# Kernel optimization log

Measured on AMD Instinct MI355X. Metric: run time of the kernel, lower is better.

Reference implementation:

```python
import jax, jax.numpy as jnp
import numpy as np

DIM = 1024
N_HEADS = 16
HEAD_DIM = DIM // N_HEADS
D_LATENT = 256
B, T = 1, 4096


def setup_inputs() -> dict:
    key = jax.random.key(0)
    ks = jax.random.split(key, 6)
    s = 0.02
    return {
        "x": jax.random.normal(ks[0], (B, T, DIM), dtype=jnp.float32),
        "W_DKV": jax.random.normal(ks[1], (DIM, D_LATENT), dtype=jnp.float32) * s,
        "W_UK": jax.random.normal(ks[2], (D_LATENT, DIM), dtype=jnp.float32) * s,
        "W_UV": jax.random.normal(ks[3], (D_LATENT, DIM), dtype=jnp.float32) * s,
        "W_UQ": jax.random.normal(ks[4], (DIM, DIM), dtype=jnp.float32) * s,
        "W_O": jax.random.normal(ks[5], (DIM, DIM), dtype=jnp.float32) * s,
    }


def reference(x, W_DKV, W_UK, W_UV, W_UQ, W_O):
    b, t, d = x.shape
    h, hd = N_HEADS, HEAD_DIM
    # low-rank latent KV projection
    c_kv = x @ W_DKV                                   # (b, t, d_latent)
    k = (c_kv @ W_UK).reshape(b, t, h, hd)             # (b, t, h, hd)
    v = (c_kv @ W_UV).reshape(b, t, h, hd)
    q = (x @ W_UQ).reshape(b, t, h, hd)
    scale = 1.0 / jnp.sqrt(jnp.asarray(hd, x.dtype))
    scores = jnp.einsum("bqhd,bkhd->bhqk", q, k) * scale   # (b, h, t, t)
    causal = jnp.tril(jnp.ones((t, t), dtype=bool))
    scores = jnp.where(causal, scores, jnp.asarray(-jnp.inf, scores.dtype))
    probs = jax.nn.softmax(scores, axis=-1)            # dropout is eval-mode identity
    ctx = jnp.einsum("bhqk,bkhd->bqhd", probs, v).reshape(b, t, d)
    return ctx @ W_O
```

## Files before the change

### kernel.cpp

```cpp
#include <hip/hip_runtime.h>
#include <hip/hip_bf16.h>
#include <stdint.h>

#define T_SEQ 4096
#define DIMX 1024
#define NH 16
#define HD 64
#define DLAT 256

typedef __bf16 bf16x8 __attribute__((ext_vector_type(8)));
typedef __bf16 bf16x4 __attribute__((ext_vector_type(4)));
typedef float floatx4 __attribute__((ext_vector_type(4)));

#define MFMA(a, b, c) __builtin_amdgcn_mfma_f32_16x16x32_bf16(a, b, c, 0, 0, 0)

__device__ inline void gload_lds16(const __bf16* g, __bf16* l) {
  __builtin_amdgcn_global_load_lds(
      (const __attribute__((address_space(1))) uint32_t*)g,
      (__attribute__((address_space(3))) uint32_t*)l, 16, 0, 0);
}

__global__ __launch_bounds__(256) void prep_kernel(
    const float* __restrict__ x, const float* __restrict__ wdkv,
    const float* __restrict__ wuk, const float* __restrict__ wuv,
    const float* __restrict__ wuq, const float* __restrict__ wo,
    __bf16* __restrict__ x_bf, __bf16* __restrict__ wt_dkv,
    __bf16* __restrict__ wt_uk, __bf16* __restrict__ wt_uv,
    __bf16* __restrict__ wt_uq, __bf16* __restrict__ wt_o) {
  int id = blockIdx.x;
  if (id < 2048) {
    int i = id * 256 + threadIdx.x;
    const float4* p = (const float4*)x;
    float4 a = p[2 * i], b = p[2 * i + 1];
    bf16x8 r = {(__bf16)a.x, (__bf16)a.y, (__bf16)a.z, (__bf16)a.w,
                (__bf16)b.x, (__bf16)b.y, (__bf16)b.z, (__bf16)b.w};
    *(bf16x8*)(x_bf + 8 * (size_t)i) = r;
    return;
  }
  int t = id - 2048;
  const float* in;
  __bf16* out;
  int R, C, lt;
  if (t < 64)       { in = wdkv; out = wt_dkv; R = 1024; C = 256;  lt = t; }
  else if (t < 128) { in = wuk;  out = wt_uk;  R = 256;  C = 1024; lt = t - 64; }
  else if (t < 192) { in = wuv;  out = wt_uv;  R = 256;  C = 1024; lt = t - 128; }
  else if (t < 448) { in = wuq;  out = wt_uq;  R = 1024; C = 1024; lt = t - 192; }
  else              { in = wo;   out = wt_o;   R = 1024; C = 1024; lt = t - 448; }
  __shared__ __bf16 tls[64][65];
  int tpr = C >> 6;
  int r0 = (lt / tpr) * 64, c0 = (lt % tpr) * 64;
  int tid = threadIdx.x;
#pragma unroll
  for (int i = 0; i < 16; i++) {
    int idx = tid + i * 256;
    int r = idx >> 6, c = idx & 63;
    tls[r][c] = (__bf16)in[(size_t)(r0 + r) * C + c0 + c];
  }
  __syncthreads();
#pragma unroll
  for (int i = 0; i < 16; i++) {
    int idx = tid + i * 256;
    int rr = idx & 63, cc = idx >> 6;
    out[(size_t)(c0 + cc) * R + r0 + rr] = tls[rr][cc];
  }
}

#define BUFE 4096

__global__ __launch_bounds__(256) void gemm_a128(const __bf16* __restrict__ A,
                                                 const __bf16* __restrict__ B1,
                                                 const __bf16* __restrict__ B2,
                                                 __bf16* __restrict__ C1,
                                                 __bf16* __restrict__ C2) {
  __shared__ __attribute__((aligned(16))) __bf16 Al[2][BUFE];
  __shared__ __attribute__((aligned(16))) __bf16 Bl[2][BUFE];
  int tid = threadIdx.x;
  int w = tid >> 6, lane = tid & 63;
  int quad = lane >> 4, l16 = lane & 15;
  int mw = w & 1, nw = w >> 1;
  int bx = blockIdx.x, m0 = blockIdx.y * 128;
  const __bf16* Bt;
  __bf16* C;
  int n0, N;
  float sc;
  if (bx < 2) { Bt = B1; C = C1; n0 = bx * 128; N = DLAT; sc = 1.0f; }
  else        { Bt = B2; C = C2; n0 = (bx - 2) * 128; N = DIMX;
                sc = 0.125f * 1.44269504088896340736f; }
  const int K = DIMX;
  int arow = w * 32 + (lane >> 2), acol = (lane & 3) << 3;

  floatx4 acc[4][4];
#pragma unroll
  for (int i = 0; i < 4; i++)
#pragma unroll
    for (int j = 0; j < 4; j++) acc[i][j] = (floatx4){0.f, 0.f, 0.f, 0.f};

  for (int k0 = 0; k0 < K; k0 += 64) {
#pragma unroll
    for (int kh = 0; kh < 2; kh++)
#pragma unroll
      for (int j = 0; j < 2; j++) {
        gload_lds16(A + (size_t)(m0 + arow + j * 16) * K + k0 + kh * 32 + acol,
                    &Al[kh][(w * 32 + j * 16) * 32]);
        gload_lds16(Bt + (size_t)(n0 + arow + j * 16) * K + k0 + kh * 32 + acol,
                    &Bl[kh][(w * 32 + j * 16) * 32]);
      }
    __syncthreads();
#pragma unroll
    for (int kh = 0; kh < 2; kh++) {
      bf16x8 af[4], bfr[4];
#pragma unroll
      for (int mt = 0; mt < 4; mt++)
        af[mt] =
            *(const bf16x8*)&Al[kh][(mw * 64 + mt * 16 + l16) * 32 + quad * 8];
#pragma unroll
      for (int nt = 0; nt < 4; nt++)
        bfr[nt] =
            *(const bf16x8*)&Bl[kh][(nw * 64 + nt * 16 + l16) * 32 + quad * 8];
#pragma unroll
      for (int mt = 0; mt < 4; mt++)
#pragma unroll
        for (int nt = 0; nt < 4; nt++)
          acc[mt][nt] = MFMA(af[mt], bfr[nt], acc[mt][nt]);
    }
    __syncthreads();
  }
#pragma unroll
  for (int mt = 0; mt < 4; mt++)
#pragma unroll
    for (int nt = 0; nt < 4; nt++)
#pragma unroll
      for (int r = 0; r < 4; r++) {
        int row = m0 + mw * 64 + mt * 16 + quad * 4 + r;
        int col = n0 + nw * 64 + nt * 16 + l16;
        C[(size_t)row * N + col] = (__bf16)(acc[mt][nt][r] * sc);
      }
}

__global__ __launch_bounds__(256) void gemm_kv128(const __bf16* __restrict__ A,
                                                  const __bf16* __restrict__ Bk,
                                                  const __bf16* __restrict__ Bv,
                                                  __bf16* __restrict__ k,
                                                  __bf16* __restrict__ vt) {
  __shared__ __attribute__((aligned(16))) __bf16 Al[2][BUFE];
  __shared__ __attribute__((aligned(16))) __bf16 Bl[2][BUFE];
  __shared__ __attribute__((aligned(16))) __bf16 tw[4][64 * 72];
  int tid = threadIdx.x;
  int w = tid >> 6, lane = tid & 63;
  int quad = lane >> 4, l16 = lane & 15;
  int mw = w & 1, nw = w >> 1;
  int bx = blockIdx.x, m0 = blockIdx.y * 128;
  bool is_k = (bx < 8);
  const __bf16* Bt = is_k ? Bk : Bv;
  int n0 = (is_k ? bx : bx - 8) * 128;
  const int K = DLAT;
  int arow = w * 32 + (lane >> 2), acol = (lane & 3) << 3;

  floatx4 acc[4][4];
#pragma unroll
  for (int i = 0; i < 4; i++)
#pragma unroll
    for (int j = 0; j < 4; j++) acc[i][j] = (floatx4){0.f, 0.f, 0.f, 0.f};

  for (int k0 = 0; k0 < K; k0 += 64) {
#pragma unroll
    for (int kh = 0; kh < 2; kh++)
#pragma unroll
      for (int j = 0; j < 2; j++) {
        gload_lds16(A + (size_t)(m0 + arow + j * 16) * K + k0 + kh * 32 + acol,
                    &Al[kh][(w * 32 + j * 16) * 32]);
        gload_lds16(Bt + (size_t)(n0 + arow + j * 16) * K + k0 + kh * 32 + acol,
                    &Bl[kh][(w * 32 + j * 16) * 32]);
      }
    __syncthreads();
#pragma unroll
    for (int kh = 0; kh < 2; kh++) {
      bf16x8 af[4], bfr[4];
#pragma unroll
      for (int mt = 0; mt < 4; mt++)
        af[mt] =
            *(const bf16x8*)&Al[kh][(mw * 64 + mt * 16 + l16) * 32 + quad * 8];
#pragma unroll
      for (int nt = 0; nt < 4; nt++)
        bfr[nt] =
            *(const bf16x8*)&Bl[kh][(nw * 64 + nt * 16 + l16) * 32 + quad * 8];
#pragma unroll
      for (int mt = 0; mt < 4; mt++)
#pragma unroll
        for (int nt = 0; nt < 4; nt++)
          acc[mt][nt] = MFMA(af[mt], bfr[nt], acc[mt][nt]);
    }
    __syncthreads();
  }
  if (is_k) {
#pragma unroll
    for (int mt = 0; mt < 4; mt++)
#pragma unroll
      for (int nt = 0; nt < 4; nt++)
#pragma unroll
        for (int r = 0; r < 4; r++) {
          int row = m0 + mw * 64 + mt * 16 + quad * 4 + r;
          int col = n0 + nw * 64 + nt * 16 + l16;
          k[(size_t)row * DIMX + col] = (__bf16)acc[mt][nt][r];
        }
  } else {
#pragma unroll
    for (int mt = 0; mt < 4; mt++)
#pragma unroll
      for (int nt = 0; nt < 4; nt++)
#pragma unroll
        for (int r = 0; r < 4; r++)
          tw[w][(nt * 16 + l16) * 72 + mt * 16 + quad * 4 + r] =
              (__bf16)acc[mt][nt][r];
    int cbase = lane >> 3, chunk = lane & 7;
#pragma unroll
    for (int i = 0; i < 8; i++) {
      int c = cbase + i * 8;
      bf16x8 v8 = *(const bf16x8*)&tw[w][c * 72 + chunk * 8];
      *(bf16x8*)&vt[(size_t)(n0 + nw * 64 + c) * T_SEQ + m0 + mw * 64 +
                    chunk * 8] = v8;
    }
  }
}

__global__ __launch_bounds__(256) void gemm_f128(const __bf16* __restrict__ A,
                                                 const __bf16* __restrict__ Bt,
                                                 float* __restrict__ C) {
  __shared__ __attribute__((aligned(16))) __bf16 Al[2][BUFE];
  __shared__ __attribute__((aligned(16))) __bf16 Bl[2][BUFE];
  int tid = threadIdx.x;
  int w = tid >> 6, lane = tid & 63;
  int quad = lane >> 4, l16 = lane & 15;
  int mw = w & 1, nw = w >> 1;
  int n0 = blockIdx.x * 128, m0 = blockIdx.y * 128;
  const int K = DIMX, N = DIMX;
  int arow = w * 32 + (lane >> 2), acol = (lane & 3) << 3;

  floatx4 acc[4][4];
#pragma unroll
  for (int i = 0; i < 4; i++)
#pragma unroll
    for (int j = 0; j < 4; j++) acc[i][j] = (floatx4){0.f, 0.f, 0.f, 0.f};

  for (int k0 = 0; k0 < K; k0 += 64) {
#pragma unroll
    for (int kh = 0; kh < 2; kh++)
#pragma unroll
      for (int j = 0; j < 2; j++) {
        gload_lds16(A + (size_t)(m0 + arow + j * 16) * K + k0 + kh * 32 + acol,
                    &Al[kh][(w * 32 + j * 16) * 32]);
        gload_lds16(Bt + (size_t)(n0 + arow + j * 16) * K + k0 + kh * 32 + acol,
                    &Bl[kh][(w * 32 + j * 16) * 32]);
      }
    __syncthreads();
#pragma unroll
    for (int kh = 0; kh < 2; kh++) {
      bf16x8 af[4], bfr[4];
#pragma unroll
      for (int mt = 0; mt < 4; mt++)
        af[mt] =
            *(const bf16x8*)&Al[kh][(mw * 64 + mt * 16 + l16) * 32 + quad * 8];
#pragma unroll
      for (int nt = 0; nt < 4; nt++)
        bfr[nt] =
            *(const bf16x8*)&Bl[kh][(nw * 64 + nt * 16 + l16) * 32 + quad * 8];
#pragma unroll
      for (int mt = 0; mt < 4; mt++)
#pragma unroll
        for (int nt = 0; nt < 4; nt++)
          acc[mt][nt] = MFMA(af[mt], bfr[nt], acc[mt][nt]);
    }
    __syncthreads();
  }
#pragma unroll
  for (int mt = 0; mt < 4; mt++)
#pragma unroll
    for (int nt = 0; nt < 4; nt++)
#pragma unroll
      for (int r = 0; r < 4; r++) {
        int row = m0 + mw * 64 + mt * 16 + quad * 4 + r;
        int col = n0 + nw * 64 + nt * 16 + l16;
        C[(size_t)row * N + col] = acc[mt][nt][r];
      }
}

#define PST 72
__global__ __launch_bounds__(256, 3) void mla_attn8(const __bf16* __restrict__ Q,
                                                    const __bf16* __restrict__ Kg,
                                                    const __bf16* __restrict__ Vt,
                                                    __bf16* __restrict__ ctx) {
  __shared__ __attribute__((aligned(16))) __bf16 Kl[2][64 * 64];
  __shared__ __attribute__((aligned(16))) __bf16 Vl[2][64 * 64];
  __shared__ __attribute__((aligned(16))) __bf16 Pl[64 * PST];
  int tid = threadIdx.x;
  int wave = tid >> 6, lane = tid & 63;
  int quad = lane >> 4, l16 = lane & 15;
  int h = blockIdx.y;
  int qt = 63 - blockIdx.x;
  int q0 = qt * 64;
  int srow = tid >> 3, pos = tid & 7;
  int gco = pos << 3;
  int sw = (pos ^ (srow & 7)) << 3;
  int swr = srow * 64 + sw;
  int fr = (wave * 16 + l16) * PST;
  int c0s = ((quad ^ (l16 & 7)) << 3);
  int c1s = (((4 + quad) ^ (l16 & 7)) << 3);

  *(bf16x8*)&Pl[srow * PST + gco] =
      *(const bf16x8*)&Q[(size_t)(q0 + srow) * DIMX + h * HD + gco];
  *(bf16x8*)&Pl[(srow + 32) * PST + gco] =
      *(const bf16x8*)&Q[(size_t)(q0 + srow + 32) * DIMX + h * HD + gco];
  *(bf16x8*)&Kl[0][swr] =
      *(const bf16x8*)&Kg[(size_t)srow * DIMX + h * HD + gco];
  *(bf16x8*)&Kl[0][swr + 2048] =
      *(const bf16x8*)&Kg[(size_t)(srow + 32) * DIMX + h * HD + gco];
  *(bf16x8*)&Vl[0][swr] =
      *(const bf16x8*)&Vt[(size_t)(h * HD + srow) * T_SEQ + gco];
  *(bf16x8*)&Vl[0][swr + 2048] =
      *(const bf16x8*)&Vt[(size_t)(h * HD + srow + 32) * T_SEQ + gco];
  __syncthreads();
  bf16x8 qf0 = *(const bf16x8*)&Pl[fr + quad * 8];
  bf16x8 qf1 = *(const bf16x8*)&Pl[fr + 32 + quad * 8];

  floatx4 o[4];
  float lsum = 0.f;
#pragma unroll
  for (int i = 0; i < 4; i++) o[i] = (floatx4){0.f, 0.f, 0.f, 0.f};

  for (int kt = 0; kt <= qt; kt++) {
    int cur = kt & 1, nxt = cur ^ 1;
    bool pre = (kt < qt);
    bf16x8 kp0, kp1, vp0, vp1;
    if (pre) {
      int k0n = (kt + 1) * 64;
      kp0 = *(const bf16x8*)&Kg[(size_t)(k0n + srow) * DIMX + h * HD + gco];
      kp1 = *(const bf16x8*)&Kg[(size_t)(k0n + srow + 32) * DIMX + h * HD + gco];
      vp0 = *(const bf16x8*)&Vt[(size_t)(h * HD + srow) * T_SEQ + k0n + gco];
      vp1 = *(const bf16x8*)&Vt[(size_t)(h * HD + srow + 32) * T_SEQ + k0n + gco];
    }
    const __bf16* Kc = Kl[cur];
    const __bf16* Vc = Vl[cur];
    floatx4 s[4];
    __builtin_amdgcn_s_setprio(1);
#pragma unroll
    for (int ct = 0; ct < 4; ct++) {
      int rb = (ct * 16 + l16) * 64;
      bf16x8 kf0 = *(const bf16x8*)&Kc[rb + c0s];
      bf16x8 kf1 = *(const bf16x8*)&Kc[rb + c1s];
      floatx4 z = (floatx4){0.f, 0.f, 0.f, 0.f};
      z = MFMA(kf0, qf0, z);
      z = MFMA(kf1, qf1, z);
      s[ct] = z;
    }
    __builtin_amdgcn_s_setprio(0);
    bool diag = (kt == qt);
#pragma unroll
    for (int ct = 0; ct < 4; ct++) {
      float p0[4];
#pragma unroll
      for (int r = 0; r < 4; r++) {
        float p = __builtin_amdgcn_exp2f(s[ct][r]);
        if (diag && (ct * 16 + quad * 4 + r > wave * 16 + l16)) p = 0.f;
        lsum += p;
        p0[r] = p;
      }
      bf16x4 pk = {(__bf16)p0[0], (__bf16)p0[1], (__bf16)p0[2], (__bf16)p0[3]};
      *(bf16x4*)&Pl[(wave * 16 + l16) * PST + ct * 16 + quad * 4] = pk;
    }
    bf16x8 pf0 = *(const bf16x8*)&Pl[fr + quad * 8];
    bf16x8 pf1 = *(const bf16x8*)&Pl[fr + 32 + quad * 8];
    __builtin_amdgcn_s_setprio(1);
#pragma unroll
    for (int dt = 0; dt < 4; dt++) {
      int rb = (dt * 16 + l16) * 64;
      bf16x8 vf0 = *(const bf16x8*)&Vc[rb + c0s];
      bf16x8 vf1 = *(const bf16x8*)&Vc[rb + c1s];
      o[dt] = MFMA(pf0, vf0, o[dt]);
      o[dt] = MFMA(pf1, vf1, o[dt]);
    }
    __builtin_amdgcn_s_setprio(0);
    if (pre) {
      *(bf16x8*)&Kl[nxt][swr] = kp0;
      *(bf16x8*)&Kl[nxt][swr + 2048] = kp1;
      *(bf16x8*)&Vl[nxt][swr] = vp0;
      *(bf16x8*)&Vl[nxt][swr + 2048] = vp1;
    }
    __syncthreads();
  }

  lsum += __shfl_xor(lsum, 16, 64);
  lsum += __shfl_xor(lsum, 32, 64);
  float inv[4];
#pragma unroll
  for (int r = 0; r < 4; r++) inv[r] = 1.0f / __shfl(lsum, quad * 4 + r, 16);

#pragma unroll
  for (int dt = 0; dt < 4; dt++)
#pragma unroll
    for (int r = 0; r < 4; r++) {
      float val = o[dt][r] * inv[r];
      int row = q0 + wave * 16 + quad * 4 + r;
      int col = h * HD + dt * 16 + l16;
      ctx[(size_t)row * DIMX + col] = (__bf16)val;
    }
}

extern "C" void kernel_launch(void* const* d_in, const int* in_sizes, int n_in,
                              void* d_out, int out_size, void* d_ws,
                              size_t ws_size, hipStream_t stream) {
  const float* x = (const float*)d_in[0];
  const float* wdkv = (const float*)d_in[1];
  const float* wuk = (const float*)d_in[2];
  const float* wuv = (const float*)d_in[3];
  const float* wuq = (const float*)d_in[4];
  const float* wo = (const float*)d_in[5];
  float* out = (float*)d_out;

  __bf16* ws = (__bf16*)d_ws;
  __bf16* x_bf = ws;
  __bf16* q = x_bf + (size_t)T_SEQ * DIMX;
  __bf16* k = q + (size_t)T_SEQ * DIMX;
  __bf16* vt = k + (size_t)T_SEQ * DIMX;
  __bf16* ctx = vt + (size_t)T_SEQ * DIMX;
  __bf16* ckv = ctx + (size_t)T_SEQ * DIMX;
  __bf16* wt_dkv = ckv + (size_t)T_SEQ * DLAT;
  __bf16* wt_uk = wt_dkv + (size_t)DLAT * DIMX;
  __bf16* wt_uv = wt_uk + (size_t)DIMX * DLAT;
  __bf16* wt_uq = wt_uv + (size_t)DIMX * DLAT;
  __bf16* wt_o = wt_uq + (size_t)DIMX * DIMX;

  dim3 blk(256);
  prep_kernel<<<dim3(2752), blk, 0, stream>>>(x, wdkv, wuk, wuv, wuq, wo, x_bf,
                                              wt_dkv, wt_uk, wt_uv, wt_uq, wt_o);
  gemm_a128<<<dim3(10, T_SEQ / 128), blk, 0, stream>>>(x_bf, wt_dkv, wt_uq,
                                                       ckv, q);
  gemm_kv128<<<dim3(16, T_SEQ / 128), blk, 0, stream>>>(ckv, wt_uk, wt_uv, k,
                                                        vt);
  mla_attn8<<<dim3(64, NH), dim3(256), 0, stream>>>(q, k, vt, ctx);
  gemm_f128<<<dim3(DIMX / 128, T_SEQ / 128), blk, 0, stream>>>(ctx, wt_o, out);
}
```

Measured before the change: 229.1 us.

## Load V fragments from global into registers and swap attention grid order

```diff
diff --git a/kernel.cpp b/kernel.cpp
--- a/kernel.cpp
+++ b/kernel.cpp
@@ -285,18 +285,17 @@
 }
 
 #define PST 72
-__global__ __launch_bounds__(256, 3) void mla_attn8(const __bf16* __restrict__ Q,
+__global__ __launch_bounds__(256, 3) void mla_attn9(const __bf16* __restrict__ Q,
                                                     const __bf16* __restrict__ Kg,
                                                     const __bf16* __restrict__ Vt,
                                                     __bf16* __restrict__ ctx) {
   __shared__ __attribute__((aligned(16))) __bf16 Kl[2][64 * 64];
-  __shared__ __attribute__((aligned(16))) __bf16 Vl[2][64 * 64];
   __shared__ __attribute__((aligned(16))) __bf16 Pl[64 * PST];
   int tid = threadIdx.x;
   int wave = tid >> 6, lane = tid & 63;
   int quad = lane >> 4, l16 = lane & 15;
-  int h = blockIdx.y;
-  int qt = 63 - blockIdx.x;
+  int h = blockIdx.x;
+  int qt = 63 - blockIdx.y;
   int q0 = qt * 64;
   int srow = tid >> 3, pos = tid & 7;
   int gco = pos << 3;
@@ -305,6 +304,7 @@
   int fr = (wave * 16 + l16) * PST;
   int c0s = ((quad ^ (l16 & 7)) << 3);
   int c1s = (((4 + quad) ^ (l16 & 7)) << 3);
+  const __bf16* vptr = Vt + (size_t)(h * HD + l16) * T_SEQ + quad * 8;
 
   *(bf16x8*)&Pl[srow * PST + gco] =
       *(const bf16x8*)&Q[(size_t)(q0 + srow) * DIMX + h * HD + gco];
@@ -314,10 +314,13 @@
       *(const bf16x8*)&Kg[(size_t)srow * DIMX + h * HD + gco];
   *(bf16x8*)&Kl[0][swr + 2048] =
       *(const bf16x8*)&Kg[(size_t)(srow + 32) * DIMX + h * HD + gco];
-  *(bf16x8*)&Vl[0][swr] =
-      *(const bf16x8*)&Vt[(size_t)(h * HD + srow) * T_SEQ + gco];
-  *(bf16x8*)&Vl[0][swr + 2048] =
-      *(const bf16x8*)&Vt[(size_t)(h * HD + srow + 32) * T_SEQ + gco];
+  bf16x8 vc[8], vn[8];
+#pragma unroll
+  for (int dt = 0; dt < 4; dt++)
+#pragma unroll
+    for (int hf = 0; hf < 2; hf++)
+      vc[dt * 2 + hf] =
+          *(const bf16x8*)&vptr[(size_t)(dt * 16) * T_SEQ + hf * 32];
   __syncthreads();
   bf16x8 qf0 = *(const bf16x8*)&Pl[fr + quad * 8];
   bf16x8 qf1 = *(const bf16x8*)&Pl[fr + 32 + quad * 8];
@@ -330,16 +333,19 @@
   for (int kt = 0; kt <= qt; kt++) {
     int cur = kt & 1, nxt = cur ^ 1;
     bool pre = (kt < qt);
-    bf16x8 kp0, kp1, vp0, vp1;
+    bf16x8 kp0, kp1;
     if (pre) {
       int k0n = (kt + 1) * 64;
       kp0 = *(const bf16x8*)&Kg[(size_t)(k0n + srow) * DIMX + h * HD + gco];
       kp1 = *(const bf16x8*)&Kg[(size_t)(k0n + srow + 32) * DIMX + h * HD + gco];
-      vp0 = *(const bf16x8*)&Vt[(size_t)(h * HD + srow) * T_SEQ + k0n + gco];
-      vp1 = *(const bf16x8*)&Vt[(size_t)(h * HD + srow + 32) * T_SEQ + k0n + gco];
+#pragma unroll
+      for (int dt = 0; dt < 4; dt++)
+#pragma unroll
+        for (int hf = 0; hf < 2; hf++)
+          vn[dt * 2 + hf] = *(const bf16x8*)&vptr[(size_t)(dt * 16) * T_SEQ +
+                                                  k0n + hf * 32];
     }
     const __bf16* Kc = Kl[cur];
-    const __bf16* Vc = Vl[cur];
     floatx4 s[4];
     __builtin_amdgcn_s_setprio(1);
 #pragma unroll
@@ -372,18 +378,15 @@
     __builtin_amdgcn_s_setprio(1);
 #pragma unroll
     for (int dt = 0; dt < 4; dt++) {
-      int rb = (dt * 16 + l16) * 64;
-      bf16x8 vf0 = *(const bf16x8*)&Vc[rb + c0s];
-      bf16x8 vf1 = *(const bf16x8*)&Vc[rb + c1s];
-      o[dt] = MFMA(pf0, vf0, o[dt]);
-      o[dt] = MFMA(pf1, vf1, o[dt]);
+      o[dt] = MFMA(pf0, vc[dt * 2 + 0], o[dt]);
+      o[dt] = MFMA(pf1, vc[dt * 2 + 1], o[dt]);
     }
     __builtin_amdgcn_s_setprio(0);
     if (pre) {
       *(bf16x8*)&Kl[nxt][swr] = kp0;
       *(bf16x8*)&Kl[nxt][swr + 2048] = kp1;
-      *(bf16x8*)&Vl[nxt][swr] = vp0;
-      *(bf16x8*)&Vl[nxt][swr + 2048] = vp1;
+#pragma unroll
+      for (int i = 0; i < 8; i++) vc[i] = vn[i];
     }
     __syncthreads();
   }
@@ -436,6 +439,6 @@
                                                        ckv, q);
   gemm_kv128<<<dim3(16, T_SEQ / 128), blk, 0, stream>>>(ckv, wt_uk, wt_uv, k,
                                                         vt);
-  mla_attn8<<<dim3(64, NH), dim3(256), 0, stream>>>(q, k, vt, ctx);
+  mla_attn9<<<dim3(NH, 64), dim3(256), 0, stream>>>(q, k, vt, ctx);
   gemm_f128<<<dim3(DIMX / 128, T_SEQ / 128), blk, 0, stream>>>(ctx, wt_o, out);
 }
```

New measurement: 280.4 us. 22.4% more time.
